# Kernel tuning notes

Hardware: AMD Instinct MI355X
Metric: run time of the kernel (lower is better)

Reference implementation:

```python
import jax, jax.numpy as jnp
import numpy as np

E, H, I = 5, 768, 1024  # num_experts, hidden_dim, intermediate_dim
TOP_K = 2


def setup_inputs() -> dict:
    key = jax.random.key(0)
    ks = jax.random.split(key, 6)
    s = 0.02
    return {
        "x": jax.random.normal(ks[0], (4, 2048, H), dtype=jnp.float32),
        "router_w": jax.random.normal(ks[1], (E, H), dtype=jnp.float32) * s,  # torch Linear (out,in)
        "router_b": jnp.zeros((E,), dtype=jnp.float32),
        "gate_w": jax.random.normal(ks[2], (E, H, I), dtype=jnp.float32) * s,
        "up_w": jax.random.normal(ks[3], (E, H, I), dtype=jnp.float32) * s,
        "down_w": jax.random.normal(ks[4], (E, I, H), dtype=jnp.float32) * s,
    }


def reference(x, router_w, router_b, gate_w, up_w, down_w):
    B, S, Hd = x.shape
    xf = x.reshape(-1, Hd)                       # [T, H]
    T = xf.shape[0]
    # Router: linear (with bias) -> softmax -> top-2 -> renormalize
    logits = xf @ router_w.T + router_b          # [T, E]
    scores = jax.nn.softmax(logits, axis=-1)
    vals, idx = jax.lax.top_k(scores, TOP_K)     # [T, 2]
    vals = vals / jnp.sum(vals, axis=-1, keepdims=True)
    # Dense combine weights: zero for unselected experts (same math as the
    # per-expert gather/scatter loop in the original module).
    comb = jnp.zeros((T, gate_w.shape[0]), dtype=x.dtype)
    comb = comb.at[jnp.arange(T)[:, None], idx].add(vals)  # [T, E]
    # SwiGLU per expert, vectorized over experts
    g = jnp.einsum('th,ehi->tei', xf, gate_w)    # [T, E, I]
    u = jnp.einsum('th,ehi->tei', xf, up_w)
    y = jnp.einsum('tei,eih->teh', jax.nn.silu(g) * u, down_w)  # [T, E, H]
    out = jnp.einsum('teh,te->th', y, comb)
    return out.reshape(B, S, Hd)
```

## Files before the change

kernel.cpp:

```cpp
#include <hip/hip_runtime.h>
#include <hip/hip_bf16.h>
#include <cstdint>
#include <cstddef>

#define T_TOK 8192
#define H_DIM 768
#define I_DIM 1024
#define N_EXP 5
#define MAXTILE 136

typedef short v8s __attribute__((ext_vector_type(8)));
typedef float v4f __attribute__((ext_vector_type(4)));

static __device__ __forceinline__ unsigned short f2bf(float f) {
    union { float f; unsigned int u; } v; v.f = f;
    unsigned int u = v.u;
    unsigned int r = (u + 0x7fffu + ((u >> 16) & 1u)) >> 16;
    return (unsigned short)r;
}
static __device__ __forceinline__ float bf2f(unsigned short s) {
    union { unsigned int u; float f; } v; v.u = ((unsigned int)s) << 16; return v.f;
}

static __device__ __forceinline__ void async16(const unsigned short* g, unsigned short* l) {
    __builtin_amdgcn_global_load_lds(
        (const __attribute__((address_space(1))) unsigned int*)g,
        (__attribute__((address_space(3))) unsigned int*)l, 16, 0, 0);
}

__global__ void k_transp_wi(const float* __restrict__ gw, const float* __restrict__ uw,
                            unsigned short* __restrict__ wbt) {
    __shared__ float tile[32][33];
    int z = blockIdx.z;
    int e = z % N_EXP;
    int isUp = z >= N_EXP;
    const float* src = (isUp ? uw : gw) + (size_t)e * H_DIM * I_DIM;
    int c0 = blockIdx.x * 32, r0 = blockIdx.y * 32;
    int tx = threadIdx.x, ty = threadIdx.y;
#pragma unroll
    for (int i = 0; i < 4; i++)
        tile[ty * 4 + i][tx] = src[(size_t)(r0 + ty * 4 + i) * I_DIM + c0 + tx];
    __syncthreads();
#pragma unroll
    for (int i = 0; i < 4; i++) {
        int c = c0 + ty * 4 + i;
        int row = (c >> 4) * 32 + (c & 15) + (isUp ? 16 : 0);
        wbt[((size_t)e * 2 * I_DIM + row) * H_DIM + r0 + tx] = f2bf(tile[tx][ty * 4 + i]);
    }
}

__global__ void k_transp_d(const float* __restrict__ dw, unsigned short* __restrict__ dbt) {
    __shared__ float tile[32][33];
    int e = blockIdx.z;
    const float* src = dw + (size_t)e * I_DIM * H_DIM;
    unsigned short* dst = dbt + (size_t)e * I_DIM * H_DIM;
    int c0 = blockIdx.x * 32, r0 = blockIdx.y * 32;
    int tx = threadIdx.x, ty = threadIdx.y;
#pragma unroll
    for (int i = 0; i < 4; i++)
        tile[ty * 4 + i][tx] = src[(size_t)(r0 + ty * 4 + i) * H_DIM + c0 + tx];
    __syncthreads();
#pragma unroll
    for (int i = 0; i < 4; i++)
        dst[(size_t)(c0 + ty * 4 + i) * I_DIM + r0 + tx] = f2bf(tile[tx][ty * 4 + i]);
}

__global__ void k_router_a(const float* __restrict__ x, const float* __restrict__ rw,
                           const float* __restrict__ rb,
                           unsigned short* __restrict__ xb,
                           int* __restrict__ top2e, float2* __restrict__ top2w) {
    const int wave = threadIdx.x >> 6, lane = threadIdx.x & 63;
    const int t = blockIdx.x * 4 + wave;
    const float* xr = x + (size_t)t * H_DIM;
    unsigned short* xbr = xb + (size_t)t * H_DIM;
    float acc[N_EXP];
#pragma unroll
    for (int e = 0; e < N_EXP; e++) acc[e] = 0.f;
#pragma unroll
    for (int j = 0; j < H_DIM / 256; j++) {
        int idx = j * 256 + lane * 4;
        float4 xv = *(const float4*)(xr + idx);
        ushort4 o;
        o.x = f2bf(xv.x); o.y = f2bf(xv.y); o.z = f2bf(xv.z); o.w = f2bf(xv.w);
        *(ushort4*)(xbr + idx) = o;
#pragma unroll
        for (int e = 0; e < N_EXP; e++) {
            float4 wv = *(const float4*)(rw + e * H_DIM + idx);
            acc[e] += xv.x * wv.x + xv.y * wv.y + xv.z * wv.z + xv.w * wv.w;
        }
    }
#pragma unroll
    for (int s = 32; s > 0; s >>= 1) {
#pragma unroll
        for (int e = 0; e < N_EXP; e++) acc[e] += __shfl_down(acc[e], s);
    }
    if (lane == 0) {
        float l[N_EXP];
#pragma unroll
        for (int e = 0; e < N_EXP; e++) l[e] = acc[e] + rb[e];
        int i1 = 0;
#pragma unroll
        for (int e = 1; e < N_EXP; e++) if (l[e] > l[i1]) i1 = e;
        int i2 = (i1 == 0) ? 1 : 0;
#pragma unroll
        for (int e = 0; e < N_EXP; e++) if (e != i1 && l[e] > l[i2]) i2 = e;
        float w1 = 1.f / (1.f + __expf(l[i2] - l[i1]));
        top2e[t] = i1 | (i2 << 8);
        top2w[t] = make_float2(w1, 1.f - w1);
    }
}

__global__ void k_router_b(const int* __restrict__ top2e, const float2* __restrict__ top2w,
                           int* __restrict__ cnt, int* __restrict__ tokslot,
                           float* __restrict__ pweight) {
    __shared__ int lcnt[N_EXP], lbase[N_EXP];
    const int tid = threadIdx.x;
    if (tid < N_EXP) lcnt[tid] = 0;
    __syncthreads();
    const int t = blockIdx.x * 256 + tid;
    const int pe = top2e[t];
    const float2 wv = top2w[t];
    const int e1 = pe & 0xff, e2 = pe >> 8;
    const int s1 = atomicAdd(&lcnt[e1], 1);
    const int s2 = atomicAdd(&lcnt[e2], 1);
    __syncthreads();
    if (tid < N_EXP) lbase[tid] = atomicAdd(&cnt[tid], lcnt[tid]);
    __syncthreads();
    const int p1 = lbase[e1] + s1;
    tokslot[e1 * T_TOK + p1] = t; pweight[e1 * T_TOK + p1] = wv.x;
    const int p2 = lbase[e2] + s2;
    tokslot[e2 * T_TOK + p2] = t | (1 << 16); pweight[e2 * T_TOK + p2] = wv.y;
}

__global__ void k_tiles(const int* __restrict__ cnt, int4* __restrict__ tiles) {
    const int tid = threadIdx.x;
    if (tid < MAXTILE) tiles[tid] = make_int4(-1, 0, 0, 0);
    __syncthreads();
    if (tid == 0) {
        int off = 0, idx = 0;
        for (int e = 0; e < N_EXP; e++) {
            int cn = cnt[e];
            for (int m0 = 0; m0 < cn; m0 += 128)
                tiles[idx++] = make_int4(e, m0, off, cn);
            off += cn;
        }
    }
}

__launch_bounds__(256, 2)
__global__ void k_gateup(const unsigned short* __restrict__ xb,
                         const unsigned short* __restrict__ wbt,
                         const int4* __restrict__ tiles,
                         const int* __restrict__ tokslot,
                         const float* __restrict__ pweight,
                         unsigned short* __restrict__ hbuf) {
    const int4 td = tiles[blockIdx.x];
    const int e = td.x;
    if (e < 0) return;
    const int m0 = td.y, offe = td.z, cn = td.w;
    const int n0 = blockIdx.y * 64;

    __shared__ __align__(16) unsigned short ldsA[128 * 32];
    __shared__ __align__(16) unsigned short ldsB[128 * 32];
    __shared__ int tokLds[128];
    __shared__ float pwLds[128];

    const int tid = threadIdx.x;
    if (tid < 128) {
        int gr = m0 + tid;
        int tk = 0; float pw = 0.f;
        if (gr < cn) { tk = tokslot[e * T_TOK + gr] & 0xFFFF; pw = pweight[e * T_TOK + gr]; }
        tokLds[tid] = tk; pwLds[tid] = pw;
    }
    __syncthreads();

    const int lane = tid & 63;
    const int wave = tid >> 6;
    const int fm = lane & 15, quad = lane >> 4;

    const int srow = wave * 16 + (lane >> 2);
    const int scol = (lane & 3) * 8;
    const unsigned short* aG1 = xb + (size_t)tokLds[srow] * H_DIM + scol;
    const unsigned short* aG2 = xb + (size_t)tokLds[64 + srow] * H_DIM + scol;
    const unsigned short* bG1 = wbt + ((size_t)e * 2 * I_DIM + n0 * 2 + srow) * H_DIM + scol;
    const unsigned short* bG2 = wbt + ((size_t)e * 2 * I_DIM + n0 * 2 + 64 + srow) * H_DIM + scol;
    unsigned short* lA1 = ldsA + wave * 512;
    unsigned short* lA2 = ldsA + 2048 + wave * 512;
    unsigned short* lB1 = ldsB + wave * 512;
    unsigned short* lB2 = ldsB + 2048 + wave * 512;

    const int wm = (wave & 1) * 64, wnw = wave >> 1;

    v4f acc[4][4];
#pragma unroll
    for (int i = 0; i < 4; i++)
#pragma unroll
        for (int j = 0; j < 4; j++) acc[i][j] = (v4f)0.f;

    for (int kb = 0; kb < H_DIM / 32; kb++) {
        const int k0 = kb * 32;
        async16(aG1 + k0, lA1);
        async16(aG2 + k0, lA2);
        async16(bG1 + k0, lB1);
        async16(bG2 + k0, lB2);
        __syncthreads();
        v8s aF[4], bF[4];
#pragma unroll
        for (int im = 0; im < 4; im++)
            aF[im] = *(const v8s*)&ldsA[(wm + im * 16 + fm) * 32 + quad * 8];
#pragma unroll
        for (int in = 0; in < 4; in++)
            bF[in] = *(const v8s*)&ldsB[(wnw * 64 + in * 16 + fm) * 32 + quad * 8];
#pragma unroll
        for (int im = 0; im < 4; im++)
#pragma unroll
            for (int in = 0; in < 4; in++)
                acc[im][in] = __builtin_amdgcn_mfma_f32_16x16x32_bf16(aF[im], bF[in], acc[im][in], 0, 0, 0);
        __syncthreads();
    }

#pragma unroll
    for (int im = 0; im < 4; im++) {
#pragma unroll
        for (int reg = 0; reg < 4; reg++) {
            int lr = wm + im * 16 + quad * 4 + reg;
            int gr = m0 + lr;
            if (gr < cn) {
                float pw = pwLds[lr];
                size_t base = (size_t)(offe + gr) * I_DIM + n0 + wnw * 32 + fm;
#pragma unroll
                for (int j = 0; j < 2; j++) {
                    float g = acc[im][2 * j][reg];
                    float u = acc[im][2 * j + 1][reg];
                    float s = g / (1.f + __expf(-g));
                    hbuf[base + j * 16] = f2bf(s * u * pw);
                }
            }
        }
    }
}

__launch_bounds__(256, 2)
__global__ void k_down(const unsigned short* __restrict__ hbuf,
                       const unsigned short* __restrict__ dbt,
                       const int4* __restrict__ tiles,
                       const int* __restrict__ tokslot,
                       unsigned short* __restrict__ ybuf) {
    const int4 td = tiles[blockIdx.x];
    const int e = td.x;
    if (e < 0) return;
    const int m0 = td.y, offe = td.z, cn = td.w;
    const int n0 = blockIdx.y * 128;

    __shared__ __align__(16) unsigned short ldsA[128 * 32];
    __shared__ __align__(16) unsigned short ldsB[128 * 32];
    __shared__ int tokLds[128];

    const int tid = threadIdx.x;
    if (tid < 128) {
        int gr = m0 + tid;
        tokLds[tid] = (gr < cn) ? tokslot[e * T_TOK + gr] : 0;
    }
    __syncthreads();

    const int lane = tid & 63;
    const int wave = tid >> 6;
    const int fm = lane & 15, quad = lane >> 4;

    const int srow = wave * 16 + (lane >> 2);
    const int scol = (lane & 3) * 8;
    int ar1 = m0 + srow;      if (ar1 >= cn) ar1 = cn - 1;
    int ar2 = m0 + 64 + srow; if (ar2 >= cn) ar2 = cn - 1;
    const unsigned short* aG1 = hbuf + (size_t)(offe + ar1) * I_DIM + scol;
    const unsigned short* aG2 = hbuf + (size_t)(offe + ar2) * I_DIM + scol;
    const unsigned short* bG1 = dbt + ((size_t)e * H_DIM + n0 + srow) * I_DIM + scol;
    const unsigned short* bG2 = dbt + ((size_t)e * H_DIM + n0 + 64 + srow) * I_DIM + scol;
    unsigned short* lA1 = ldsA + wave * 512;
    unsigned short* lA2 = ldsA + 2048 + wave * 512;
    unsigned short* lB1 = ldsB + wave * 512;
    unsigned short* lB2 = ldsB + 2048 + wave * 512;

    const int wm = (wave & 1) * 64, wn = (wave >> 1) * 64;

    v4f acc[4][4];
#pragma unroll
    for (int i = 0; i < 4; i++)
#pragma unroll
        for (int j = 0; j < 4; j++) acc[i][j] = (v4f)0.f;

    for (int kb = 0; kb < I_DIM / 32; kb++) {
        const int k0 = kb * 32;
        async16(aG1 + k0, lA1);
        async16(aG2 + k0, lA2);
        async16(bG1 + k0, lB1);
        async16(bG2 + k0, lB2);
        __syncthreads();
        v8s aF[4], bF[4];
#pragma unroll
        for (int im = 0; im < 4; im++)
            aF[im] = *(const v8s*)&ldsA[(wm + im * 16 + fm) * 32 + quad * 8];
#pragma unroll
        for (int in = 0; in < 4; in++)
            bF[in] = *(const v8s*)&ldsB[(wn + in * 16 + fm) * 32 + quad * 8];
#pragma unroll
        for (int im = 0; im < 4; im++)
#pragma unroll
            for (int in = 0; in < 4; in++)
                acc[im][in] = __builtin_amdgcn_mfma_f32_16x16x32_bf16(aF[im], bF[in], acc[im][in], 0, 0, 0);
        __syncthreads();
    }

#pragma unroll
    for (int im = 0; im < 4; im++) {
#pragma unroll
        for (int reg = 0; reg < 4; reg++) {
            int lr = wm + im * 16 + quad * 4 + reg;
            int gr = m0 + lr;
            if (gr < cn) {
                int v = tokLds[lr];
                int tok = v & 0xFFFF, s = (v >> 16) & 1;
#pragma unroll
                for (int in = 0; in < 4; in++) {
                    int col = n0 + wn + in * 16 + fm;
                    ybuf[((size_t)s * T_TOK + tok) * H_DIM + col] = f2bf(acc[im][in][reg]);
                }
            }
        }
    }
}

__global__ void k_combine(const unsigned short* __restrict__ ybuf, float* __restrict__ out) {
    const size_t i8 = ((size_t)blockIdx.x * 256 + threadIdx.x) * 8;
    const unsigned short* y0 = ybuf + i8;
    const unsigned short* y1 = ybuf + (size_t)T_TOK * H_DIM + i8;
    ushort4 a0 = *(const ushort4*)y0, a1 = *(const ushort4*)(y0 + 4);
    ushort4 b0 = *(const ushort4*)y1, b1 = *(const ushort4*)(y1 + 4);
    float4 o0, o1;
    o0.x = bf2f(a0.x) + bf2f(b0.x); o0.y = bf2f(a0.y) + bf2f(b0.y);
    o0.z = bf2f(a0.z) + bf2f(b0.z); o0.w = bf2f(a0.w) + bf2f(b0.w);
    o1.x = bf2f(a1.x) + bf2f(b1.x); o1.y = bf2f(a1.y) + bf2f(b1.y);
    o1.z = bf2f(a1.z) + bf2f(b1.z); o1.w = bf2f(a1.w) + bf2f(b1.w);
    *(float4*)(out + i8) = o0;
    *(float4*)(out + i8 + 4) = o1;
}

extern "C" void kernel_launch(void* const* d_in, const int* in_sizes, int n_in,
                              void* d_out, int out_size, void* d_ws, size_t ws_size,
                              hipStream_t stream) {
    const float* x  = (const float*)d_in[0];
    const float* rw = (const float*)d_in[1];
    const float* rb = (const float*)d_in[2];
    const float* gw = (const float*)d_in[3];
    const float* uw = (const float*)d_in[4];
    const float* dw = (const float*)d_in[5];
    float* out = (float*)d_out;

    char* ws = (char*)d_ws;
    size_t o = 0;
    auto alloc = [&](size_t bytes) { void* p = ws + o; o += (bytes + 255) & ~255ull; return p; };
    int*   cnt     = (int*)  alloc(N_EXP * 4);
    int*   tokslot = (int*)  alloc((size_t)N_EXP * T_TOK * 4);
    float* pweight = (float*)alloc((size_t)N_EXP * T_TOK * 4);
    int*   top2e   = (int*)  alloc((size_t)T_TOK * 4);
    float2* top2w  = (float2*)alloc((size_t)T_TOK * 8);
    int4*  tiles   = (int4*) alloc((size_t)MAXTILE * 16);
    unsigned short* xb   = (unsigned short*)alloc((size_t)T_TOK * H_DIM * 2);
    unsigned short* wbt  = (unsigned short*)alloc((size_t)N_EXP * 2 * I_DIM * H_DIM * 2);
    unsigned short* dbt  = (unsigned short*)alloc((size_t)N_EXP * H_DIM * I_DIM * 2);
    unsigned short* hbuf = (unsigned short*)alloc((size_t)2 * T_TOK * I_DIM * 2);
    unsigned short* ybuf = (unsigned short*)alloc((size_t)2 * T_TOK * H_DIM * 2);

    hipMemsetAsync(cnt, 0, N_EXP * 4, stream);

    dim3 tg1(I_DIM / 32, H_DIM / 32, 2 * N_EXP);
    k_transp_wi<<<tg1, dim3(32, 8), 0, stream>>>(gw, uw, wbt);
    dim3 tg2(H_DIM / 32, I_DIM / 32, N_EXP);
    k_transp_d<<<tg2, dim3(32, 8), 0, stream>>>(dw, dbt);

    k_router_a<<<T_TOK / 4, 256, 0, stream>>>(x, rw, rb, xb, top2e, top2w);
    k_router_b<<<T_TOK / 256, 256, 0, stream>>>(top2e, top2w, cnt, tokslot, pweight);
    k_tiles<<<1, 256, 0, stream>>>(cnt, tiles);

    dim3 g1(MAXTILE, I_DIM / 64);
    k_gateup<<<g1, 256, 0, stream>>>(xb, wbt, tiles, tokslot, pweight, hbuf);

    dim3 g2(MAXTILE, H_DIM / 128);
    k_down<<<g2, 256, 0, stream>>>(hbuf, dbt, tiles, tokslot, ybuf);

    k_combine<<<(T_TOK * H_DIM) / (256 * 8), 256, 0, stream>>>(ybuf, out);
}
```

Measured before the change: 265.9 us.

## Merge weight transposes, vectorize them, swizzle LDS columns, raise occupancy bounds

The two weight-transpose kernels are merged into one launch that reads with float4 and writes ushort4, replacing scalar accesses. Both GEMM kernels apply an XOR-style rotation to the 8-element column chunk used for global-to-LDS copies and for fragment reads, to cut LDS bank conflicts. Launch bounds rise from 2 to 4 blocks per CU, which caps register use and may cause spills. The hbuf allocation is padded by 128 rows. The merged transpose grid is sized for the larger dimension, so some blocks exit early without work.

```diff
diff --git a/kernel.cpp b/kernel.cpp
--- a/kernel.cpp
+++ b/kernel.cpp
@@ -28,41 +28,45 @@
         (__attribute__((address_space(3))) unsigned int*)l, 16, 0, 0);
 }
 
-__global__ void k_transp_wi(const float* __restrict__ gw, const float* __restrict__ uw,
-                            unsigned short* __restrict__ wbt) {
+__global__ void k_transp_all(const float* __restrict__ gw, const float* __restrict__ uw,
+                             const float* __restrict__ dw,
+                             unsigned short* __restrict__ wbt, unsigned short* __restrict__ dbt) {
     __shared__ float tile[32][33];
-    int z = blockIdx.z;
-    int e = z % N_EXP;
-    int isUp = z >= N_EXP;
-    const float* src = (isUp ? uw : gw) + (size_t)e * H_DIM * I_DIM;
-    int c0 = blockIdx.x * 32, r0 = blockIdx.y * 32;
-    int tx = threadIdx.x, ty = threadIdx.y;
-#pragma unroll
-    for (int i = 0; i < 4; i++)
-        tile[ty * 4 + i][tx] = src[(size_t)(r0 + ty * 4 + i) * I_DIM + c0 + tx];
-    __syncthreads();
-#pragma unroll
-    for (int i = 0; i < 4; i++) {
-        int c = c0 + ty * 4 + i;
-        int row = (c >> 4) * 32 + (c & 15) + (isUp ? 16 : 0);
-        wbt[((size_t)e * 2 * I_DIM + row) * H_DIM + r0 + tx] = f2bf(tile[tx][ty * 4 + i]);
-    }
-}
-
-__global__ void k_transp_d(const float* __restrict__ dw, unsigned short* __restrict__ dbt) {
-    __shared__ float tile[32][33];
-    int e = blockIdx.z;
-    const float* src = dw + (size_t)e * I_DIM * H_DIM;
-    unsigned short* dst = dbt + (size_t)e * I_DIM * H_DIM;
-    int c0 = blockIdx.x * 32, r0 = blockIdx.y * 32;
-    int tx = threadIdx.x, ty = threadIdx.y;
-#pragma unroll
-    for (int i = 0; i < 4; i++)
-        tile[ty * 4 + i][tx] = src[(size_t)(r0 + ty * 4 + i) * H_DIM + c0 + tx];
-    __syncthreads();
-#pragma unroll
-    for (int i = 0; i < 4; i++)
-        dst[(size_t)(c0 + ty * 4 + i) * I_DIM + r0 + tx] = f2bf(tile[tx][ty * 4 + i]);
+    const int z = blockIdx.z;
+    const int tid = threadIdx.x;
+    const int row = tid >> 3, cq = tid & 7;
+    const int ocol = tid >> 3, seg = tid & 7;
+    if (z < 2 * N_EXP) {
+        if (blockIdx.y >= H_DIM / 32) return;
+        const int e = z % N_EXP;
+        const int isUp = z >= N_EXP;
+        const float* src = (isUp ? uw : gw) + (size_t)e * H_DIM * I_DIM;
+        const int c0 = blockIdx.x * 32, r0 = blockIdx.y * 32;
+        float4 v = *(const float4*)(src + (size_t)(r0 + row) * I_DIM + c0 + cq * 4);
+        tile[row][cq * 4 + 0] = v.x; tile[row][cq * 4 + 1] = v.y;
+        tile[row][cq * 4 + 2] = v.z; tile[row][cq * 4 + 3] = v.w;
+        __syncthreads();
+        int c = c0 + ocol;
+        int orow = (c >> 4) * 32 + (c & 15) + (isUp ? 16 : 0);
+        ushort4 o;
+        o.x = f2bf(tile[seg * 4 + 0][ocol]); o.y = f2bf(tile[seg * 4 + 1][ocol]);
+        o.z = f2bf(tile[seg * 4 + 2][ocol]); o.w = f2bf(tile[seg * 4 + 3][ocol]);
+        *(ushort4*)(wbt + ((size_t)e * 2 * I_DIM + orow) * H_DIM + r0 + seg * 4) = o;
+    } else {
+        if (blockIdx.x >= H_DIM / 32) return;
+        const int e = z - 2 * N_EXP;
+        const float* src = dw + (size_t)e * I_DIM * H_DIM;
+        unsigned short* dst = dbt + (size_t)e * I_DIM * H_DIM;
+        const int c0 = blockIdx.x * 32, r0 = blockIdx.y * 32;
+        float4 v = *(const float4*)(src + (size_t)(r0 + row) * H_DIM + c0 + cq * 4);
+        tile[row][cq * 4 + 0] = v.x; tile[row][cq * 4 + 1] = v.y;
+        tile[row][cq * 4 + 2] = v.z; tile[row][cq * 4 + 3] = v.w;
+        __syncthreads();
+        ushort4 o;
+        o.x = f2bf(tile[seg * 4 + 0][ocol]); o.y = f2bf(tile[seg * 4 + 1][ocol]);
+        o.z = f2bf(tile[seg * 4 + 2][ocol]); o.w = f2bf(tile[seg * 4 + 3][ocol]);
+        *(ushort4*)(dst + (size_t)(c0 + ocol) * I_DIM + r0 + seg * 4) = o;
+    }
 }
 
 __global__ void k_router_a(const float* __restrict__ x, const float* __restrict__ rw,
@@ -147,7 +151,7 @@
     }
 }
 
-__launch_bounds__(256, 2)
+__launch_bounds__(256, 4)
 __global__ void k_gateup(const unsigned short* __restrict__ xb,
                          const unsigned short* __restrict__ wbt,
                          const int4* __restrict__ tiles,
@@ -177,13 +181,14 @@
     const int lane = tid & 63;
     const int wave = tid >> 6;
     const int fm = lane & 15, quad = lane >> 4;
+    const int pq = (quad + (fm >> 1)) & 3;
 
     const int srow = wave * 16 + (lane >> 2);
-    const int scol = (lane & 3) * 8;
+    const int scol = (((lane & 3) - (srow >> 1)) & 3) * 8;
     const unsigned short* aG1 = xb + (size_t)tokLds[srow] * H_DIM + scol;
     const unsigned short* aG2 = xb + (size_t)tokLds[64 + srow] * H_DIM + scol;
     const unsigned short* bG1 = wbt + ((size_t)e * 2 * I_DIM + n0 * 2 + srow) * H_DIM + scol;
-    const unsigned short* bG2 = wbt + ((size_t)e * 2 * I_DIM + n0 * 2 + 64 + srow) * H_DIM + scol;
+    const unsigned short* bG2 = bG1 + (size_t)64 * H_DIM;
     unsigned short* lA1 = ldsA + wave * 512;
     unsigned short* lA2 = ldsA + 2048 + wave * 512;
     unsigned short* lB1 = ldsB + wave * 512;
@@ -207,10 +212,10 @@
         v8s aF[4], bF[4];
 #pragma unroll
         for (int im = 0; im < 4; im++)
-            aF[im] = *(const v8s*)&ldsA[(wm + im * 16 + fm) * 32 + quad * 8];
+            aF[im] = *(const v8s*)&ldsA[(wm + im * 16 + fm) * 32 + pq * 8];
 #pragma unroll
         for (int in = 0; in < 4; in++)
-            bF[in] = *(const v8s*)&ldsB[(wnw * 64 + in * 16 + fm) * 32 + quad * 8];
+            bF[in] = *(const v8s*)&ldsB[(wnw * 64 + in * 16 + fm) * 32 + pq * 8];
 #pragma unroll
         for (int im = 0; im < 4; im++)
 #pragma unroll
@@ -240,7 +245,7 @@
     }
 }
 
-__launch_bounds__(256, 2)
+__launch_bounds__(256, 4)
 __global__ void k_down(const unsigned short* __restrict__ hbuf,
                        const unsigned short* __restrict__ dbt,
                        const int4* __restrict__ tiles,
@@ -266,15 +271,16 @@
     const int lane = tid & 63;
     const int wave = tid >> 6;
     const int fm = lane & 15, quad = lane >> 4;
+    const int pq = (quad + (fm >> 1)) & 3;
 
     const int srow = wave * 16 + (lane >> 2);
-    const int scol = (lane & 3) * 8;
+    const int scol = (((lane & 3) - (srow >> 1)) & 3) * 8;
     int ar1 = m0 + srow;      if (ar1 >= cn) ar1 = cn - 1;
     int ar2 = m0 + 64 + srow; if (ar2 >= cn) ar2 = cn - 1;
     const unsigned short* aG1 = hbuf + (size_t)(offe + ar1) * I_DIM + scol;
     const unsigned short* aG2 = hbuf + (size_t)(offe + ar2) * I_DIM + scol;
     const unsigned short* bG1 = dbt + ((size_t)e * H_DIM + n0 + srow) * I_DIM + scol;
-    const unsigned short* bG2 = dbt + ((size_t)e * H_DIM + n0 + 64 + srow) * I_DIM + scol;
+    const unsigned short* bG2 = bG1 + (size_t)64 * I_DIM;
     unsigned short* lA1 = ldsA + wave * 512;
     unsigned short* lA2 = ldsA + 2048 + wave * 512;
     unsigned short* lB1 = ldsB + wave * 512;
@@ -298,10 +304,10 @@
         v8s aF[4], bF[4];
 #pragma unroll
         for (int im = 0; im < 4; im++)
-            aF[im] = *(const v8s*)&ldsA[(wm + im * 16 + fm) * 32 + quad * 8];
+            aF[im] = *(const v8s*)&ldsA[(wm + im * 16 + fm) * 32 + pq * 8];
 #pragma unroll
         for (int in = 0; in < 4; in++)
-            bF[in] = *(const v8s*)&ldsB[(wn + in * 16 + fm) * 32 + quad * 8];
+            bF[in] = *(const v8s*)&ldsB[(wn + in * 16 + fm) * 32 + pq * 8];
 #pragma unroll
         for (int im = 0; im < 4; im++)
 #pragma unroll
@@ -358,24 +364,22 @@
     char* ws = (char*)d_ws;
     size_t o = 0;
     auto alloc = [&](size_t bytes) { void* p = ws + o; o += (bytes + 255) & ~255ull; return p; };
-    int*   cnt     = (int*)  alloc(N_EXP * 4);
-    int*   tokslot = (int*)  alloc((size_t)N_EXP * T_TOK * 4);
-    float* pweight = (float*)alloc((size_t)N_EXP * T_TOK * 4);
-    int*   top2e   = (int*)  alloc((size_t)T_TOK * 4);
-    float2* top2w  = (float2*)alloc((size_t)T_TOK * 8);
-    int4*  tiles   = (int4*) alloc((size_t)MAXTILE * 16);
+    int*    cnt     = (int*)   alloc(N_EXP * 4);
+    int*    tokslot = (int*)   alloc((size_t)N_EXP * T_TOK * 4);
+    float*  pweight = (float*) alloc((size_t)N_EXP * T_TOK * 4);
+    int*    top2e   = (int*)   alloc((size_t)T_TOK * 4);
+    float2* top2w   = (float2*)alloc((size_t)T_TOK * 8);
+    int4*   tiles   = (int4*)  alloc((size_t)MAXTILE * 16);
     unsigned short* xb   = (unsigned short*)alloc((size_t)T_TOK * H_DIM * 2);
     unsigned short* wbt  = (unsigned short*)alloc((size_t)N_EXP * 2 * I_DIM * H_DIM * 2);
     unsigned short* dbt  = (unsigned short*)alloc((size_t)N_EXP * H_DIM * I_DIM * 2);
-    unsigned short* hbuf = (unsigned short*)alloc((size_t)2 * T_TOK * I_DIM * 2);
+    unsigned short* hbuf = (unsigned short*)alloc((size_t)(2 * T_TOK + 128) * I_DIM * 2);
     unsigned short* ybuf = (unsigned short*)alloc((size_t)2 * T_TOK * H_DIM * 2);
 
     hipMemsetAsync(cnt, 0, N_EXP * 4, stream);
 
-    dim3 tg1(I_DIM / 32, H_DIM / 32, 2 * N_EXP);
-    k_transp_wi<<<tg1, dim3(32, 8), 0, stream>>>(gw, uw, wbt);
-    dim3 tg2(H_DIM / 32, I_DIM / 32, N_EXP);
-    k_transp_d<<<tg2, dim3(32, 8), 0, stream>>>(dw, dbt);
+    dim3 tg(I_DIM / 32, I_DIM / 32, 3 * N_EXP);
+    k_transp_all<<<tg, 256, 0, stream>>>(gw, uw, dw, wbt, dbt);
 
     k_router_a<<<T_TOK / 4, 256, 0, stream>>>(x, rw, rb, xb, top2e, top2w);
     k_router_b<<<T_TOK / 256, 256, 0, stream>>>(top2e, top2w, cnt, tokslot, pweight);
```

After: 264.0 us. No clear change (-0.7%).
